# Performance work log

Measured on AMD Instinct MI355X. Metric: run time of the kernel, lower is better.

## Reference

```python
import jax, jax.numpy as jnp
import numpy as np

B, D, L, N = 16, 256, 4096, 4096
MAX_SPAN = 64


def setup_inputs() -> dict:
    key = jax.random.key(0)
    k1, k2, k3 = jax.random.split(key, 3)
    features = jax.random.normal(k1, (B, D, L), dtype=jnp.float32)
    # TOI spans: start in [0, L - MAX_SPAN), length in [1, MAX_SPAN]
    start = jax.random.randint(k2, (B, N), 0, L - MAX_SPAN, dtype=jnp.int32)
    length = jax.random.randint(k3, (B, N), 1, MAX_SPAN + 1, dtype=jnp.int32)
    tois = jnp.stack([start, start + length], axis=-1)  # [B, N, 2]
    return {"features": features, "tois": tois}


def _pool_one(feat, toi):
    # feat: [D, L], toi: [N, 2] -> [N, 3*D]
    start = toi[:, 0]
    end = toi[:, 1]
    # cumsum with zero-padding column: [D, L+1]
    cs = jnp.concatenate(
        [jnp.zeros((feat.shape[0], 1), dtype=feat.dtype), jnp.cumsum(feat, axis=1)],
        axis=1,
    )
    span_len = (end - start).astype(feat.dtype)
    avg = (cs[:, end] - cs[:, start]) / span_len          # [D, N]
    head = feat[:, start]                                  # [D, N]
    tail = feat[:, end - 1]                                # [D, N]
    return jnp.concatenate([head, avg, tail], axis=0).T    # [N, 3*D]


def reference(features, tois):
    # features: [B, D, L] float32, tois: [B, N, 2] int32
    pooled = jax.vmap(_pool_one)(features, tois)           # [B, N, 3*D]
    out = pooled.reshape(-1, pooled.shape[-1])             # [B*N, 3*D]
    n = tois.shape[1]
    counts = jnp.cumsum(jnp.full((tois.shape[0],), n, dtype=jnp.int32))
    return out, counts
```

## Files before the change

kernel.cpp:

```cpp
#include <hip/hip_runtime.h>
#include <hip/hip_bf16.h>

constexpr int B = 16;
constexpr int D = 256;
constexpr int L = 4096;
constexpr int N = 4096;
constexpr int TS = 64;
constexpr int NT = L / TS;

typedef float v4f __attribute__((ext_vector_type(4)));

__global__ __launch_bounds__(256) void row_scan(const float* __restrict__ feat,
                                                float* __restrict__ P,
                                                float* __restrict__ cs_t) {
    __shared__ float tsum[NT];
    int row = blockIdx.x;
    int tid = threadIdx.x;
    const float4* fr = (const float4*)(feat + (size_t)row * L);

    float s[4];
    #pragma unroll
    for (int r = 0; r < 4; ++r) {
        float4 v = fr[r * 256 + tid];
        s[r] = (v.x + v.y) + (v.z + v.w);
    }
    #pragma unroll
    for (int r = 0; r < 4; ++r) {
        float v = s[r];
        #pragma unroll
        for (int off = 1; off < 16; off <<= 1) v += __shfl_xor(v, off, 64);
        if ((tid & 15) == 0) tsum[r * 16 + (tid >> 4)] = v;
    }
    __syncthreads();

    if (tid < NT) {
        float v = tsum[tid];
        float incl = v;
        #pragma unroll
        for (int off = 1; off < 64; off <<= 1) {
            float u = __shfl_up(incl, off, 64);
            if (tid >= off) incl += u;
        }
        P[row * NT + tid] = incl - v;
        if (tid == NT - 1) {
            int b = row >> 8, d = row & 255;
            cs_t[((size_t)b * (L + 1) + L) * D + d] = incl;
        }
    }
}

__global__ __launch_bounds__(256) void transpose_scan(const float* __restrict__ feat,
                                                      const float* __restrict__ P,
                                                      float* __restrict__ cs_t) {
    __shared__ float tile[64][65];
    __shared__ float poff[64];
    int bid = blockIdx.x;
    int t   = bid & 63;
    int dt  = (bid >> 6) & 3;
    int b   = bid >> 8;
    int tid = threadIdx.x;
    int ll  = tid & 63;
    int k0  = tid >> 6;
    int d0  = dt * 64;
    int l0  = t * TS;

    if (tid < 64) poff[tid] = P[(b * D + d0 + tid) * NT + t];
    #pragma unroll
    for (int k = 0; k < 16; ++k) {
        int dd = k0 + k * 4;
        tile[dd][ll] = feat[((size_t)(b * D + d0 + dd)) * L + l0 + ll];
    }
    __syncthreads();

    #pragma unroll
    for (int r = 0; r < 16; ++r) {
        int dd = k0 * 16 + r;
        float v = tile[dd][ll];
        float incl = v;
        #pragma unroll
        for (int off = 1; off < 64; off <<= 1) {
            float u = __shfl_up(incl, off, 64);
            if (ll >= off) incl += u;
        }
        tile[dd][ll] = (incl - v) + poff[dd];
    }
    __syncthreads();

    #pragma unroll
    for (int k = 0; k < 16; ++k) {
        int l = k0 + k * 4;
        cs_t[((size_t)b * (L + 1) + l0 + l) * D + d0 + ll] = tile[ll][l];
    }
}

__global__ __launch_bounds__(256) void pool_queries(const float* __restrict__ cs_t,
                                                    const int* __restrict__ tois,
                                                    float* __restrict__ out) {
    int gw   = (blockIdx.x * blockDim.x + threadIdx.x) >> 6;
    int lane = threadIdx.x & 63;
    int b = gw >> 12;
    int2 se = ((const int2*)tois)[gw];
    int s = se.x, e = se.y;

    const size_t base = (size_t)b * (L + 1);
    const v4f* r_s = (const v4f*)(cs_t + (base + s) * D);
    const v4f* r_e = (const v4f*)(cs_t + (base + e) * D);

    v4f cs0 = r_s[lane];
    v4f cs1 = r_s[lane + 64];
    v4f ce1 = r_e[lane - 64];
    v4f ce0 = r_e[lane];

    float inv = 1.0f / (float)(e - s);
    v4f head = cs1 - cs0;
    v4f avg  = (ce0 - cs0) * inv;
    v4f tail = ce0 - ce1;

    v4f* orow = (v4f*)(out + (size_t)gw * (3 * D));
    __builtin_nontemporal_store(head, orow + lane);
    __builtin_nontemporal_store(avg,  orow + 64 + lane);
    __builtin_nontemporal_store(tail, orow + 128 + lane);

    if (gw == 0 && lane < B)
        out[(size_t)B * N * (3 * D) + lane] = (float)((lane + 1) * N);
}

__global__ __launch_bounds__(256) void pool_direct(const float* __restrict__ feat,
                                                   const int* __restrict__ tois,
                                                   float* __restrict__ out) {
    int gw   = (blockIdx.x * blockDim.x + threadIdx.x) >> 6;
    int lane = threadIdx.x & 63;
    if (gw >= B * N) return;
    int b = gw >> 12;
    int s = tois[gw * 2 + 0];
    int e = tois[gw * 2 + 1];
    float inv = 1.0f / (float)(e - s);
    float* orow = out + (size_t)gw * (3 * D);
    #pragma unroll
    for (int c = 0; c < 4; ++c) {
        int d = c * 64 + lane;
        const float* f = feat + ((size_t)(b * D + d)) * L;
        float sum = 0.f;
        for (int j = s; j < e; ++j) sum += f[j];
        orow[d]         = f[s];
        orow[D + d]     = sum * inv;
        orow[2 * D + d] = f[e - 1];
    }
    if (gw == 0 && lane < B)
        out[(size_t)B * N * (3 * D) + lane] = (float)((lane + 1) * N);
}

extern "C" void kernel_launch(void* const* d_in, const int* in_sizes, int n_in,
                              void* d_out, int out_size, void* d_ws, size_t ws_size,
                              hipStream_t stream) {
    const float* feat = (const float*)d_in[0];
    const int*   tois = (const int*)d_in[1];
    float*       out  = (float*)d_out;

    const size_t cs_elems = (size_t)B * (L + 1) * D;
    const size_t p_elems  = (size_t)B * D * NT;
    const size_t need     = (cs_elems + p_elems) * sizeof(float);

    if (ws_size >= need) {
        float* cs_t = (float*)d_ws;
        float* P    = cs_t + cs_elems;

        row_scan<<<B * D, 256, 0, stream>>>(feat, P, cs_t);
        transpose_scan<<<B * (D / 64) * NT, 256, 0, stream>>>(feat, P, cs_t);
        pool_queries<<<B * N / 4, 256, 0, stream>>>(cs_t, tois, out);
    } else {
        pool_direct<<<B * N / 4, 256, 0, stream>>>(feat, tois, out);
    }
}
```

Measured before the change: 292.3 us.

## Fuse row scan and transpose scan with decoupled look-back prefix

Replaces the two-pass scan (a row-total kernel followed by a transpose-scan kernel) with a single kernel. Each tile computes its local scan, publishes its aggregate and inclusive prefix through flags in global memory, and looks back over predecessor tiles to get its offset. This avoids reading the feature tensor twice and removes one launch. In exchange it adds a flag-init kernel, spin-waiting on inter-block flags, and a dependence on blocks being scheduled in order; a bounded spin guard is used to avoid hangs.

```diff
diff --git a/kernel.cpp b/kernel.cpp
--- a/kernel.cpp
+++ b/kernel.cpp
@@ -7,89 +7,114 @@
 constexpr int N = 4096;
 constexpr int TS = 64;
 constexpr int NT = L / TS;
+constexpr int NCHAIN = B * (D / 64);
 
 typedef float v4f __attribute__((ext_vector_type(4)));
 
-__global__ __launch_bounds__(256) void row_scan(const float* __restrict__ feat,
-                                                float* __restrict__ P,
-                                                float* __restrict__ cs_t) {
-    __shared__ float tsum[NT];
-    int row = blockIdx.x;
-    int tid = threadIdx.x;
-    const float4* fr = (const float4*)(feat + (size_t)row * L);
-
-    float s[4];
-    #pragma unroll
-    for (int r = 0; r < 4; ++r) {
-        float4 v = fr[r * 256 + tid];
-        s[r] = (v.x + v.y) + (v.z + v.w);
-    }
-    #pragma unroll
-    for (int r = 0; r < 4; ++r) {
-        float v = s[r];
+__global__ __launch_bounds__(256) void init_flags(int* __restrict__ flags) {
+    int i = blockIdx.x * 256 + threadIdx.x;
+    if (i < NCHAIN * NT) flags[i] = 0;
+}
+
+__global__ __launch_bounds__(256) void scan_transpose(
+        const float* __restrict__ feat,
+        float* __restrict__ cs_t,
+        float* __restrict__ aggP,
+        float* __restrict__ prefP,
+        int* __restrict__ flags) {
+    __shared__ float tile[64][65];
+    __shared__ float aggs[64];
+    __shared__ float poff[64];
+
+    const int bid   = blockIdx.x;
+    const int t     = bid & (NT - 1);
+    const int chain = bid >> 6;
+    const int dt    = chain & 3;
+    const int b     = chain >> 2;
+    const int d0    = dt * 64;
+    const int l0    = t * TS;
+    const int tid   = threadIdx.x;
+
+    {
+        int j     = tid & 15;
+        int dbase = tid >> 4;
         #pragma unroll
-        for (int off = 1; off < 16; off <<= 1) v += __shfl_xor(v, off, 64);
-        if ((tid & 15) == 0) tsum[r * 16 + (tid >> 4)] = v;
+        for (int r = 0; r < 4; ++r) {
+            int dd = dbase + r * 16;
+            const float* p = feat + (size_t)(b * D + d0 + dd) * L + l0 + 4 * j;
+            float4 v = *(const float4*)p;
+            tile[dd][4 * j + 0] = v.x;
+            tile[dd][4 * j + 1] = v.y;
+            tile[dd][4 * j + 2] = v.z;
+            tile[dd][4 * j + 3] = v.w;
+        }
     }
     __syncthreads();
 
-    if (tid < NT) {
-        float v = tsum[tid];
-        float incl = v;
+    {
+        int ll = tid & 63, w = tid >> 6;
         #pragma unroll
-        for (int off = 1; off < 64; off <<= 1) {
-            float u = __shfl_up(incl, off, 64);
-            if (tid >= off) incl += u;
-        }
-        P[row * NT + tid] = incl - v;
-        if (tid == NT - 1) {
-            int b = row >> 8, d = row & 255;
-            cs_t[((size_t)b * (L + 1) + L) * D + d] = incl;
-        }
-    }
-}
-
-__global__ __launch_bounds__(256) void transpose_scan(const float* __restrict__ feat,
-                                                      const float* __restrict__ P,
-                                                      float* __restrict__ cs_t) {
-    __shared__ float tile[64][65];
-    __shared__ float poff[64];
-    int bid = blockIdx.x;
-    int t   = bid & 63;
-    int dt  = (bid >> 6) & 3;
-    int b   = bid >> 8;
-    int tid = threadIdx.x;
-    int ll  = tid & 63;
-    int k0  = tid >> 6;
-    int d0  = dt * 64;
-    int l0  = t * TS;
-
-    if (tid < 64) poff[tid] = P[(b * D + d0 + tid) * NT + t];
-    #pragma unroll
-    for (int k = 0; k < 16; ++k) {
-        int dd = k0 + k * 4;
-        tile[dd][ll] = feat[((size_t)(b * D + d0 + dd)) * L + l0 + ll];
+        for (int r = 0; r < 16; ++r) {
+            int dd = w * 16 + r;
+            float v = tile[dd][ll];
+            float incl = v;
+            #pragma unroll
+            for (int off = 1; off < 64; off <<= 1) {
+                float u = __shfl_up(incl, off, 64);
+                if (ll >= off) incl += u;
+            }
+            tile[dd][ll] = incl - v;
+            if (ll == 63) aggs[dd] = incl;
+        }
     }
     __syncthreads();
 
-    #pragma unroll
-    for (int r = 0; r < 16; ++r) {
-        int dd = k0 * 16 + r;
-        float v = tile[dd][ll];
-        float incl = v;
+    if (tid < 64) {
+        const int d = tid;
+        const float agg = aggs[d];
+        const size_t sidx = (size_t)chain * NT + t;
+
+        if (t > 0) {
+            aggP[sidx * 64 + d] = agg;
+            __threadfence();
+            if (d == 0)
+                __hip_atomic_store(&flags[sidx], 1, __ATOMIC_RELEASE,
+                                   __HIP_MEMORY_SCOPE_AGENT);
+        }
+
+        float run = 0.f;
+        for (int tt = t - 1; tt >= 0; --tt) {
+            const size_t pidx = (size_t)chain * NT + tt;
+            int f, guard = 0;
+            do {
+                f = __hip_atomic_load(&flags[pidx], __ATOMIC_ACQUIRE,
+                                      __HIP_MEMORY_SCOPE_AGENT);
+            } while (f == 0 && ++guard < (1 << 22));
+            if (f == 2) { run += prefP[pidx * 64 + d]; break; }
+            run += aggP[pidx * 64 + d];
+        }
+
+        if (t < NT - 1) {
+            prefP[sidx * 64 + d] = run + agg;
+            __threadfence();
+            if (d == 0)
+                __hip_atomic_store(&flags[sidx], 2, __ATOMIC_RELEASE,
+                                   __HIP_MEMORY_SCOPE_AGENT);
+        } else {
+            cs_t[((size_t)b * (L + 1) + L) * D + d0 + d] = run + agg;
+        }
+        poff[d] = run;
+    }
+    __syncthreads();
+
+    {
+        int ll = tid & 63, w = tid >> 6;
         #pragma unroll
-        for (int off = 1; off < 64; off <<= 1) {
-            float u = __shfl_up(incl, off, 64);
-            if (ll >= off) incl += u;
-        }
-        tile[dd][ll] = (incl - v) + poff[dd];
-    }
-    __syncthreads();
-
-    #pragma unroll
-    for (int k = 0; k < 16; ++k) {
-        int l = k0 + k * 4;
-        cs_t[((size_t)b * (L + 1) + l0 + l) * D + d0 + ll] = tile[ll][l];
+        for (int k = 0; k < 16; ++k) {
+            int l = w + k * 4;
+            cs_t[((size_t)b * (L + 1) + l0 + l) * D + d0 + ll] =
+                tile[ll][l] + poff[ll];
+        }
     }
 }
 
@@ -157,16 +182,19 @@
     const int*   tois = (const int*)d_in[1];
     float*       out  = (float*)d_out;
 
-    const size_t cs_elems = (size_t)B * (L + 1) * D;
-    const size_t p_elems  = (size_t)B * D * NT;
-    const size_t need     = (cs_elems + p_elems) * sizeof(float);
+    const size_t cs_elems   = (size_t)B * (L + 1) * D;
+    const size_t agg_elems  = (size_t)NCHAIN * NT * 64;
+    const size_t flag_elems = (size_t)NCHAIN * NT;
+    const size_t need = (cs_elems + 2 * agg_elems + flag_elems) * sizeof(float);
 
     if (ws_size >= need) {
-        float* cs_t = (float*)d_ws;
-        float* P    = cs_t + cs_elems;
-
-        row_scan<<<B * D, 256, 0, stream>>>(feat, P, cs_t);
-        transpose_scan<<<B * (D / 64) * NT, 256, 0, stream>>>(feat, P, cs_t);
+        float* cs_t  = (float*)d_ws;
+        float* aggP  = cs_t + cs_elems;
+        float* prefP = aggP + agg_elems;
+        int*   flags = (int*)(prefP + agg_elems);
+
+        init_flags<<<(NCHAIN * NT + 255) / 256, 256, 0, stream>>>(flags);
+        scan_transpose<<<NCHAIN * NT, 256, 0, stream>>>(feat, cs_t, aggP, prefP, flags);
         pool_queries<<<B * N / 4, 256, 0, stream>>>(cs_t, tois, out);
     } else {
         pool_direct<<<B * N / 4, 256, 0, stream>>>(feat, tois, out);
```

After: 1.005 ms. +244.0%, slower.
